# Kernel tuning notes

Hardware: AMD Instinct MI355X
Metric: run time of the kernel (lower is better)

The kernel has to match this reference:

```python
import jax, jax.numpy as jnp
import numpy as np

B, T, C = 2, 2048, 1024
N_HEAD = 16
HEAD_DIM = C // N_HEAD
ROPE_BASE = 10000.0


def setup_inputs() -> dict:
    key = jax.random.key(0)
    ks = jax.random.split(key, 5)
    s = 0.02
    return {
        "x": jax.random.normal(ks[0], (B, T, C), dtype=jnp.float32),
        "Wq": jax.random.normal(ks[1], (C, C), dtype=jnp.float32) * s,
        "Wk": jax.random.normal(ks[2], (C, C), dtype=jnp.float32) * s,
        "Wv": jax.random.normal(ks[3], (C, C), dtype=jnp.float32) * s,
        "Wo": jax.random.normal(ks[4], (C, C), dtype=jnp.float32) * s,
    }


def _rope_cos_sin(seq_len, head_dim, dtype):
    inv_freq = 1.0 / (ROPE_BASE ** (jnp.arange(0, head_dim, 2, dtype=jnp.float32) / head_dim))
    t = jnp.arange(seq_len, dtype=jnp.float32)
    freqs = jnp.einsum("i,j->ij", t, inv_freq)          # [T, head_dim/2]
    emb = jnp.concatenate([freqs, freqs], axis=-1)        # [T, head_dim]
    return jnp.cos(emb).astype(dtype), jnp.sin(emb).astype(dtype)


def _rotate_half(x):
    x1, x2 = jnp.split(x, 2, axis=-1)
    return jnp.concatenate([-x2, x1], axis=-1)


def _mha(x, Wq, Wk, Wv, Wo):
    b, t, c = x.shape
    # torch nn.Linear stores weight [out, in]: y = x @ W.T
    q = (x @ Wq.T).reshape(b, t, N_HEAD, HEAD_DIM).transpose(0, 2, 1, 3)  # [B,H,T,D]
    k = (x @ Wk.T).reshape(b, t, N_HEAD, HEAD_DIM).transpose(0, 2, 1, 3)
    v = (x @ Wv.T).reshape(b, t, N_HEAD, HEAD_DIM).transpose(0, 2, 1, 3)
    cos, sin = _rope_cos_sin(t, HEAD_DIM, x.dtype)        # [T,D] each, broadcast over B,H
    q = q * cos + _rotate_half(q) * sin
    k = k * cos + _rotate_half(k) * sin
    scale = 1.0 / np.sqrt(HEAD_DIM).astype(np.float32)
    att = jnp.einsum("bhqd,bhkd->bhqk", q, k) * scale     # [B,H,T,T]
    causal = jnp.tril(jnp.ones((t, t), dtype=bool))
    att = jnp.where(causal, att, jnp.finfo(att.dtype).min)
    att = jax.nn.softmax(att, axis=-1)
    y = jnp.einsum("bhqk,bhkd->bhqd", att, v)             # [B,H,T,D]
    y = y.transpose(0, 2, 1, 3).reshape(b, t, c)
    return y @ Wo.T


def reference(x, Wq, Wk, Wv, Wo):
    return _mha(x, Wq, Wk, Wv, Wo)
```

## Files before the change

kernel.cpp:

```cpp
#include <hip/hip_runtime.h>

#define BB 2
#define TT 2048
#define CC 1024
#define NH 16
#define HD 64

typedef __attribute__((ext_vector_type(8))) short bf16x8;
typedef __attribute__((ext_vector_type(4))) float floatx4;
typedef __attribute__((ext_vector_type(16))) float floatx16;

__device__ __forceinline__ unsigned short f2bf(float f) {
    union { float f; unsigned int u; } v; v.f = f;
    unsigned int u = v.u;
    u = (u + 0x7fffu + ((u >> 16) & 1u)) >> 16;
    return (unsigned short)u;
}
__device__ __forceinline__ float bf2f(unsigned short u) {
    return __uint_as_float((unsigned)u << 16);
}

typedef __attribute__((address_space(3))) unsigned char* lds_ptr_t;
typedef const __attribute__((address_space(1))) unsigned char* glob_ptr_t;
__device__ __forceinline__ void gll16(const void* g, void* l) {
    __builtin_amdgcn_global_load_lds((glob_ptr_t)g, (lds_ptr_t)l, 16, 0, 0);
}

__global__ __launch_bounds__(256) void cast_all_k(const float* __restrict__ x,
                                                  const float* __restrict__ wq,
                                                  const float* __restrict__ wk,
                                                  const float* __restrict__ wv,
                                                  const float* __restrict__ wo,
                                                  unsigned short* __restrict__ xb,
                                                  unsigned short* __restrict__ wqkvb,
                                                  unsigned short* __restrict__ wob,
                                                  float2* __restrict__ tabQ,
                                                  float2* __restrict__ tabK) {
    if (blockIdx.x >= 8192) {
        int idx = (blockIdx.x - 8192) * 256 + threadIdx.x;
        int t = idx >> 5, j = idx & 31;
        const float C1 = 0.41524101186092f;
        const float I2PI = 0.15915494309189535f;
        float rev = (float)t * (__builtin_amdgcn_exp2f(-(float)j * C1) * I2PI);
        rev -= floorf(rev);
        float ang = rev * 6.2831853071796f;
        float c = __cosf(ang), s = __sinf(ang);
        const float qs = 0.18033688011112f;
        tabK[idx] = make_float2(c, s);
        tabQ[idx] = make_float2(c * qs, s * qs);
        return;
    }
    int i = blockIdx.x * 256 + threadIdx.x;
    const float* src;
    unsigned short* dst;
    if (i < 1048576) {
        src = x + (size_t)i * 4;
        dst = xb + (size_t)i * 4;
    } else {
        int w   = (i - 1048576) >> 18;
        int off = (i - 1048576) & 262143;
        const float* s0 = (w == 0) ? wq : (w == 1) ? wk : (w == 2) ? wv : wo;
        unsigned short* d0 = (w == 3) ? wob : (wqkvb + (size_t)w * 1048576);
        src = s0 + (size_t)off * 4;
        dst = d0 + (size_t)off * 4;
    }
    float4 v = *(const float4*)src;
    ushort4 o;
    o.x = f2bf(v.x); o.y = f2bf(v.y); o.z = f2bf(v.z); o.w = f2bf(v.w);
    *(ushort4*)dst = o;
}

__global__ __launch_bounds__(256, 2) void gemm_o_k(const unsigned short* __restrict__ A,
                                                   const unsigned short* __restrict__ Bt,
                                                   float* __restrict__ C, int N, int K) {
    __shared__ __align__(16) unsigned short As[128][64];
    __shared__ __align__(16) unsigned short Bs[64][64];
    const int tid  = threadIdx.x;
    const int wave = tid >> 6;
    const int lane = tid & 63;
    const int quad = lane >> 4;
    const int l16  = lane & 15;
    const int sw   = l16 & 7;
    const int wr = (wave >> 1) * 64;
    const int wc = (wave & 1) * 32;
    const int bid = blockIdx.x;
    const int xcd = bid & 7, sl = bid >> 3;
    const int row0 = (xcd * 4 + (sl >> 4)) * 128;
    const int col0 = (sl & 15) * 64;
    const int w8r = wave * 8 + (lane >> 3);
    const int cg  = ((lane & 7) ^ (lane >> 3)) * 8;
    const int cl  = (lane & 7) * 8;

    const unsigned short* Ap = A  + (size_t)(row0 + w8r) * K + cg;
    const unsigned short* Bp = Bt + (size_t)(col0 + w8r) * K + cg;

    floatx4 acc[4][2];
    #pragma unroll
    for (int i = 0; i < 4; i++)
        #pragma unroll
        for (int j = 0; j < 2; j++) acc[i][j] = (floatx4){0.f, 0.f, 0.f, 0.f};

    for (int k0 = 0; k0 < K; k0 += 64) {
        __syncthreads();
        #pragma unroll
        for (int isu = 0; isu < 4; isu++)
            gll16(Ap + (size_t)(isu * 32) * K + k0, &As[isu * 32 + w8r][cl]);
        #pragma unroll
        for (int isu = 0; isu < 2; isu++)
            gll16(Bp + (size_t)(isu * 32) * K + k0, &Bs[isu * 32 + w8r][cl]);
        __syncthreads();
        #pragma unroll
        for (int kk = 0; kk < 2; kk++) {
            bf16x8 af[4], bfr[2];
            #pragma unroll
            for (int i = 0; i < 4; i++)
                af[i]  = *(const bf16x8*)&As[wr + 16 * i + l16][((kk * 4 + quad) ^ sw) * 8];
            #pragma unroll
            for (int j = 0; j < 2; j++)
                bfr[j] = *(const bf16x8*)&Bs[wc + 16 * j + l16][((kk * 4 + quad) ^ sw) * 8];
            #pragma unroll
            for (int i = 0; i < 4; i++)
                #pragma unroll
                for (int j = 0; j < 2; j++)
                    acc[i][j] = __builtin_amdgcn_mfma_f32_16x16x32_bf16(af[i], bfr[j], acc[i][j], 0, 0, 0);
        }
    }

    #pragma unroll
    for (int i = 0; i < 4; i++)
        #pragma unroll
        for (int j = 0; j < 2; j++)
            #pragma unroll
            for (int r = 0; r < 4; r++) {
                int row = row0 + wr + 16 * i + quad * 4 + r;
                int col = col0 + wc + 16 * j + l16;
                C[(size_t)row * N + col] = acc[i][j][r];
            }
}

__global__ __launch_bounds__(256) void gemm_qkv_k(const unsigned short* __restrict__ A,
                                                  const unsigned short* __restrict__ Bt,
                                                  const float2* __restrict__ tabQ,
                                                  const float2* __restrict__ tabK,
                                                  unsigned short* __restrict__ Qb,
                                                  unsigned short* __restrict__ Kb,
                                                  unsigned short* __restrict__ Vb) {
    __shared__ __align__(16) unsigned short SMEM[128 * 128];
    unsigned short (*As)[64] = (unsigned short(*)[64])SMEM;
    unsigned short (*Bs)[64] = (unsigned short(*)[64])(SMEM + 128 * 64);
    unsigned short (*Eb)[128] = (unsigned short(*)[128])SMEM;
    const int K = 1024;
    const int tid  = threadIdx.x;
    const int wave = tid >> 6;
    const int lane = tid & 63;
    const int quad = lane >> 4;
    const int l16  = lane & 15;
    const int sw   = l16 & 7;
    const int wr = (wave >> 1) * 64;
    const int wc = (wave & 1) * 64;
    const int bid = blockIdx.x;
    const int xcd = bid & 7, sl = bid >> 3;
    const int row0 = (xcd * 4 + sl / 24) * 128;
    const int col0 = (sl % 24) * 128;
    const int w8r = wave * 8 + (lane >> 3);
    const int cg  = ((lane & 7) ^ (lane >> 3)) * 8;
    const int cl  = (lane & 7) * 8;

    const unsigned short* Ap = A  + (size_t)(row0 + w8r) * K + cg;
    const unsigned short* Bp = Bt + (size_t)(col0 + w8r) * K + cg;

    floatx4 acc[4][4];
    #pragma unroll
    for (int i = 0; i < 4; i++)
        #pragma unroll
        for (int j = 0; j < 4; j++) acc[i][j] = (floatx4){0.f, 0.f, 0.f, 0.f};

    for (int k0 = 0; k0 < K; k0 += 64) {
        __syncthreads();
        #pragma unroll
        for (int isu = 0; isu < 4; isu++) {
            gll16(Ap + (size_t)(isu * 32) * K + k0, &As[isu * 32 + w8r][cl]);
            gll16(Bp + (size_t)(isu * 32) * K + k0, &Bs[isu * 32 + w8r][cl]);
        }
        __syncthreads();
        #pragma unroll
        for (int kk = 0; kk < 2; kk++) {
            bf16x8 af[4], bfr[4];
            #pragma unroll
            for (int i = 0; i < 4; i++)
                af[i]  = *(const bf16x8*)&As[wr + 16 * i + l16][((kk * 4 + quad) ^ sw) * 8];
            #pragma unroll
            for (int j = 0; j < 4; j++)
                bfr[j] = *(const bf16x8*)&Bs[wc + 16 * j + l16][((kk * 4 + quad) ^ sw) * 8];
            #pragma unroll
            for (int i = 0; i < 4; i++)
                #pragma unroll
                for (int j = 0; j < 4; j++)
                    acc[i][j] = __builtin_amdgcn_mfma_f32_16x16x32_bf16(af[i], bfr[j], acc[i][j], 0, 0, 0);
        }
    }

    __syncthreads();
    #pragma unroll
    for (int i = 0; i < 4; i++)
        #pragma unroll
        for (int j = 0; j < 4; j++)
            #pragma unroll
            for (int r = 0; r < 4; r++) {
                int erow = wr + 16 * i + quad * 4 + r;
                int col  = wc + 16 * j + l16;
                int pcol = (((col >> 3) ^ (erow & 15)) << 3) | (col & 7);
                Eb[erow][pcol] = f2bf(acc[i][j][r]);
            }
    __syncthreads();

    const int row  = tid >> 1;
    const int half = tid & 1;
    const int grow = row0 + row;
    const int t    = grow & (TT - 1);
    const int bb   = grow >> 11;
    const int sect = col0 >> 10;
    const int hh   = ((col0 & 1023) >> 6) + half;
    union { int4 q[8]; unsigned short u[64]; } raw;
    #pragma unroll
    for (int i = 0; i < 8; i++) {
        int pg = (half * 8 + i) ^ (row & 15);
        raw.q[i] = *(const int4*)&Eb[row][pg << 3];
    }
    size_t obase = ((size_t)(bb * NH + hh) * TT + t) * 64;
    if (sect == 2) {
        #pragma unroll
        for (int i = 0; i < 8; i++) *(int4*)(Vb + obase + 8 * i) = raw.q[i];
    } else {
        const float4* tab = (const float4*)((sect ? tabK : tabQ) + (size_t)t * 32);
        unsigned short* dst = sect ? Kb : Qb;
        union { int4 q[8]; unsigned short u[64]; } o;
        #pragma unroll
        for (int i = 0; i < 16; i++) {
            float4 cs = tab[i];
            int j0 = 2 * i, j1 = 2 * i + 1;
            float a0 = bf2f(raw.u[j0]), b0 = bf2f(raw.u[j0 + 32]);
            float a1 = bf2f(raw.u[j1]), b1 = bf2f(raw.u[j1 + 32]);
            o.u[j0]      = f2bf(a0 * cs.x - b0 * cs.y);
            o.u[j0 + 32] = f2bf(b0 * cs.x + a0 * cs.y);
            o.u[j1]      = f2bf(a1 * cs.z - b1 * cs.w);
            o.u[j1 + 32] = f2bf(b1 * cs.z + a1 * cs.w);
        }
        #pragma unroll
        for (int i = 0; i < 8; i++) *(int4*)(dst + obase + 8 * i) = o.q[i];
    }
}

__global__ __launch_bounds__(256) void vtr_k(const unsigned short* __restrict__ Vb,
                                             unsigned short* __restrict__ Vt) {
    __shared__ __align__(16) unsigned short Vsh[64][70];
    const int tid = threadIdx.x;
    const int tt = blockIdx.x;
    const int bh = blockIdx.y;
    const int sr = tid >> 2;
    const int sc = (tid & 3) * 16;
    const unsigned short* src = Vb + ((size_t)bh * TT + tt * 64 + sr) * 64 + sc;
    *(int4*)&Vsh[sr][sc]     = *(const int4*)src;
    *(int4*)&Vsh[sr][sc + 8] = *(const int4*)(src + 8);
    __syncthreads();
    const int dr = tid >> 2;
    const int tc = (tid & 3) * 16;
    unsigned short tv[16];
    #pragma unroll
    for (int i = 0; i < 16; i++) {
        int x = tc + i;
        int key = (x & ~15) + (x & 3) + ((x >> 2) & 1) * 8 + ((x >> 3) & 1) * 4;
        tv[i] = Vsh[key][dr];
    }
    size_t vo = ((size_t)bh * 64 + dr) * TT + tt * 64 + tc;
    *(int4*)(Vt + vo)     = *(int4*)&tv[0];
    *(int4*)(Vt + vo + 8) = *(int4*)&tv[8];
}

__global__ __launch_bounds__(256, 4) void flash_k(const unsigned short* __restrict__ Qb,
                                                  const unsigned short* __restrict__ Kb,
                                                  const unsigned short* __restrict__ Vt,
                                                  unsigned short* __restrict__ O0,
                                                  unsigned short* __restrict__ O1,
                                                  float* __restrict__ L0, float* __restrict__ L1) {
    __shared__ __align__(16) unsigned short Ks[64][72];
    __shared__ __align__(16) unsigned short Vs[64][72];
    const int tid  = threadIdx.x;
    const int wave = tid >> 6;
    const int lane = tid & 63;
    const int h    = lane >> 5;
    const int l32  = lane & 31;
    const int qt    = 15 - (blockIdx.x >> 6);
    const int inner = blockIdx.x & 63;
    const int bh    = inner >> 1;
    const int split = inner & 1;
    const int q0 = qt * 128;
    const int qw = q0 + wave * 32 + l32;
    const int sr = tid >> 2;
    const int sc = (tid & 3) * 16;

    bf16x8 qf[4];
    {
        const unsigned short* qp = Qb + ((size_t)bh * TT + qw) * 64 + h * 8;
        #pragma unroll
        for (int kk = 0; kk < 4; kk++) qf[kk] = *(const bf16x8*)(qp + kk * 16);
    }

    floatx16 accO[2];
    accO[0] = (floatx16)(0.f);
    accO[1] = (floatx16)(0.f);
    float lsum = 0.f;

    const int kt0 = split * (qt + 1);
    const int kt1 = kt0 + qt + 1;
    const unsigned short* kbase = Kb + (size_t)bh * TT * 64;
    const unsigned short* vbase = Vt + (size_t)bh * 64 * TT;

    const unsigned short* kp = kbase + ((size_t)(kt0 * 64) + sr) * 64 + sc;
    const unsigned short* vp = vbase + (size_t)sr * TT + kt0 * 64 + sc;
    int4 ka = *(const int4*)kp, kb2 = *(const int4*)(kp + 8);
    int4 va = *(const int4*)vp, vb2 = *(const int4*)(vp + 8);

    for (int kt = kt0; kt < kt1; kt++) {
        __syncthreads();
        *(int4*)&Ks[sr][sc]     = ka;
        *(int4*)&Ks[sr][sc + 8] = kb2;
        *(int4*)&Vs[sr][sc]     = va;
        *(int4*)&Vs[sr][sc + 8] = vb2;
        __syncthreads();
        if (kt + 1 < kt1) {
            const unsigned short* kp2 = kbase + ((size_t)((kt + 1) * 64) + sr) * 64 + sc;
            const unsigned short* vp2 = vbase + (size_t)sr * TT + (kt + 1) * 64 + sc;
            ka  = *(const int4*)kp2; kb2 = *(const int4*)(kp2 + 8);
            va  = *(const int4*)vp2; vb2 = *(const int4*)(vp2 + 8);
        }

        const bool diag = (kt >= 2 * qt);
        bf16x8 pfrag[4];

        #pragma unroll
        for (int mb = 0; mb < 2; mb++) {
            floatx16 sacc = (floatx16)(0.f);
            __builtin_amdgcn_s_setprio(1);
            #pragma unroll
            for (int kk = 0; kk < 4; kk++) {
                bf16x8 kf = *(const bf16x8*)&Ks[32 * mb + l32][kk * 16 + h * 8];
                sacc = __builtin_amdgcn_mfma_f32_32x32x16_bf16(kf, qf[kk], sacc, 0, 0, 0);
            }
            __builtin_amdgcn_s_setprio(0);
            float p[16];
            const int kmb = kt * 64 + 32 * mb + 4 * h;
            #pragma unroll
            for (int r = 0; r < 16; r++) {
                float pv = __builtin_amdgcn_exp2f(sacc[r]);
                if (diag) {
                    int ki = kmb + (r & 3) + 8 * (r >> 2);
                    if (ki > qw) pv = 0.f;
                }
                lsum += pv;
                p[r] = pv;
            }
            #pragma unroll
            for (int half = 0; half < 2; half++) {
                union { bf16x8 v; unsigned u[4]; } pk;
                #pragma unroll
                for (int i = 0; i < 4; i++) {
                    unsigned ulo = __float_as_uint(p[half * 8 + 2 * i]);
                    unsigned uhi = __float_as_uint(p[half * 8 + 2 * i + 1]);
                    pk.u[i] = (ulo >> 16) | (uhi & 0xffff0000u);
                }
                pfrag[2 * mb + half] = pk.v;
            }
        }

        __builtin_amdgcn_s_setprio(1);
        #pragma unroll
        for (int mbo = 0; mbo < 2; mbo++) {
            #pragma unroll
            for (int kk = 0; kk < 4; kk++) {
                bf16x8 vf = *(const bf16x8*)&Vs[32 * mbo + l32][kk * 16 + h * 8];
                accO[mbo] = __builtin_amdgcn_mfma_f32_32x32x16_bf16(vf, pfrag[kk], accO[mbo], 0, 0, 0);
            }
        }
        __builtin_amdgcn_s_setprio(0);
    }

    lsum += __shfl_xor(lsum, 32);
    unsigned short* Op = split ? O1 : O0;
    float* Lp = split ? L1 : L0;
    if (lane < 32) Lp[(size_t)bh * TT + qw] = lsum;
    unsigned short* orow = Op + ((size_t)bh * TT + qw) * 64;
    #pragma unroll
    for (int mbo = 0; mbo < 2; mbo++)
        #pragma unroll
        for (int a = 0; a < 4; a++) {
            ushort4 o4;
            o4.x = f2bf(accO[mbo][4 * a + 0]);
            o4.y = f2bf(accO[mbo][4 * a + 1]);
            o4.z = f2bf(accO[mbo][4 * a + 2]);
            o4.w = f2bf(accO[mbo][4 * a + 3]);
            *(ushort4*)(orow + 32 * mbo + 8 * a + 4 * h) = o4;
        }
}

__global__ __launch_bounds__(256) void combine_k(const unsigned short* __restrict__ O0,
                                                 const unsigned short* __restrict__ O1,
                                                 const float* __restrict__ L0,
                                                 const float* __restrict__ L1,
                                                 unsigned short* __restrict__ Yb) {
    int idx = blockIdx.x * 256 + threadIdx.x;
    int dg  = idx & 15;
    int row = idx >> 4;
    float inv = 1.0f / (L0[row] + L1[row]);
    uint2 a = ((const uint2*)O0)[idx];
    uint2 b = ((const uint2*)O1)[idx];
    float a0 = __uint_as_float(a.x << 16),      b0 = __uint_as_float(b.x << 16);
    float a1 = __uint_as_float(a.x & 0xffff0000u), b1 = __uint_as_float(b.x & 0xffff0000u);
    float a2 = __uint_as_float(a.y << 16),      b2 = __uint_as_float(b.y << 16);
    float a3 = __uint_as_float(a.y & 0xffff0000u), b3 = __uint_as_float(b.y & 0xffff0000u);
    ushort4 o;
    o.x = f2bf((a0 + b0) * inv);
    o.y = f2bf((a1 + b1) * inv);
    o.z = f2bf((a2 + b2) * inv);
    o.w = f2bf((a3 + b3) * inv);
    int bh = row >> 11, t = row & (TT - 1);
    int bb = bh >> 4, hh = bh & 15;
    *(ushort4*)(Yb + ((size_t)(bb * TT + t)) * CC + hh * 64 + dg * 4) = o;
}

extern "C" void kernel_launch(void* const* d_in, const int* in_sizes, int n_in,
                              void* d_out, int out_size, void* d_ws, size_t ws_size,
                              hipStream_t stream) {
    (void)in_sizes; (void)n_in; (void)out_size; (void)ws_size;
    const float* x  = (const float*)d_in[0];
    const float* Wq = (const float*)d_in[1];
    const float* Wk = (const float*)d_in[2];
    const float* Wv = (const float*)d_in[3];
    const float* Wo = (const float*)d_in[4];
    float* out = (float*)d_out;
    char* ws = (char*)d_ws;

    unsigned short* xb    = (unsigned short*)(ws + 0);
    unsigned short* wqkvb = (unsigned short*)(ws + (8ull  << 20));
    unsigned short* wob   = (unsigned short*)(ws + (14ull << 20));
    unsigned short* Qb    = (unsigned short*)(ws + (16ull << 20));
    unsigned short* Kb    = (unsigned short*)(ws + (24ull << 20));
    unsigned short* Vb    = (unsigned short*)(ws + (32ull << 20));
    unsigned short* Vt    = (unsigned short*)(ws + (40ull << 20));
    unsigned short* Yb    = (unsigned short*)(ws + (48ull << 20));
    unsigned short* O0    = (unsigned short*)(ws + (56ull << 20));
    unsigned short* O1    = (unsigned short*)(ws + (64ull << 20));
    float* L0 = (float*)(ws + (72ull << 20));
    float* L1 = (float*)(ws + (72ull << 20) + (256ull << 10));
    float2* tabQ = (float2*)(ws + (73ull << 20));
    float2* tabK = (float2*)(ws + (73ull << 20) + (512ull << 10));

    cast_all_k<<<8448, 256, 0, stream>>>(x, Wq, Wk, Wv, Wo, xb, wqkvb, wob, tabQ, tabK);
    gemm_qkv_k<<<768, 256, 0, stream>>>(xb, wqkvb, tabQ, tabK, Qb, Kb, Vb);
    vtr_k<<<dim3(32, 32), 256, 0, stream>>>(Vb, Vt);
    flash_k<<<1024, 256, 0, stream>>>(Qb, Kb, Vt, O0, O1, L0, L1);
    combine_k<<<4096, 256, 0, stream>>>(O0, O1, L0, L1, Yb);
    gemm_o_k<<<512, 256, 0, stream>>>(Yb, wob, out, 1024, 1024);
}
```

Measured before the change: 177.6 us.

## Double-buffer K/V tiles in flash kernel, use hardware bf16 pack, widen combine

The flash kernel now keeps two K/V shared-memory buffers. The next tile is written into the alternate buffer after the compute, so each iteration needs one barrier instead of two. P-fragment packing switches from truncation bit-masking to the v_cvt_pk_bf16_f32 instruction, which rounds instead of truncating. The combine kernel processes 8 bf16 elements per thread with 128-bit loads and stores, at half the grid size. Doubling LDS use (about 36KB per block) may reduce occupancy at launch bounds of 4 blocks.

```diff
diff --git a/kernel.cpp b/kernel.cpp
--- a/kernel.cpp
+++ b/kernel.cpp
@@ -283,8 +283,8 @@
                                                   unsigned short* __restrict__ O0,
                                                   unsigned short* __restrict__ O1,
                                                   float* __restrict__ L0, float* __restrict__ L1) {
-    __shared__ __align__(16) unsigned short Ks[64][72];
-    __shared__ __align__(16) unsigned short Vs[64][72];
+    __shared__ __align__(16) unsigned short Ks[2][64][72];
+    __shared__ __align__(16) unsigned short Vs[2][64][72];
     const int tid  = threadIdx.x;
     const int wave = tid >> 6;
     const int lane = tid & 63;
@@ -316,19 +316,23 @@
     const unsigned short* kbase = Kb + (size_t)bh * TT * 64;
     const unsigned short* vbase = Vt + (size_t)bh * 64 * TT;
 
-    const unsigned short* kp = kbase + ((size_t)(kt0 * 64) + sr) * 64 + sc;
-    const unsigned short* vp = vbase + (size_t)sr * TT + kt0 * 64 + sc;
-    int4 ka = *(const int4*)kp, kb2 = *(const int4*)(kp + 8);
-    int4 va = *(const int4*)vp, vb2 = *(const int4*)(vp + 8);
-
+    {
+        const unsigned short* kp = kbase + ((size_t)(kt0 * 64) + sr) * 64 + sc;
+        const unsigned short* vp = vbase + (size_t)sr * TT + kt0 * 64 + sc;
+        int4 ka = *(const int4*)kp, kb2 = *(const int4*)(kp + 8);
+        int4 va = *(const int4*)vp, vb2 = *(const int4*)(vp + 8);
+        *(int4*)&Ks[0][sr][sc]     = ka;
+        *(int4*)&Ks[0][sr][sc + 8] = kb2;
+        *(int4*)&Vs[0][sr][sc]     = va;
+        *(int4*)&Vs[0][sr][sc + 8] = vb2;
+    }
+    __syncthreads();
+
+    int cur = 0;
     for (int kt = kt0; kt < kt1; kt++) {
-        __syncthreads();
-        *(int4*)&Ks[sr][sc]     = ka;
-        *(int4*)&Ks[sr][sc + 8] = kb2;
-        *(int4*)&Vs[sr][sc]     = va;
-        *(int4*)&Vs[sr][sc + 8] = vb2;
-        __syncthreads();
-        if (kt + 1 < kt1) {
+        int4 ka, kb2, va, vb2;
+        const bool more = (kt + 1 < kt1);
+        if (more) {
             const unsigned short* kp2 = kbase + ((size_t)((kt + 1) * 64) + sr) * 64 + sc;
             const unsigned short* vp2 = vbase + (size_t)sr * TT + (kt + 1) * 64 + sc;
             ka  = *(const int4*)kp2; kb2 = *(const int4*)(kp2 + 8);
@@ -344,30 +348,31 @@
             __builtin_amdgcn_s_setprio(1);
             #pragma unroll
             for (int kk = 0; kk < 4; kk++) {
-                bf16x8 kf = *(const bf16x8*)&Ks[32 * mb + l32][kk * 16 + h * 8];
+                bf16x8 kf = *(const bf16x8*)&Ks[cur][32 * mb + l32][kk * 16 + h * 8];
                 sacc = __builtin_amdgcn_mfma_f32_32x32x16_bf16(kf, qf[kk], sacc, 0, 0, 0);
             }
             __builtin_amdgcn_s_setprio(0);
-            float p[16];
             const int kmb = kt * 64 + 32 * mb + 4 * h;
             #pragma unroll
-            for (int r = 0; r < 16; r++) {
-                float pv = __builtin_amdgcn_exp2f(sacc[r]);
-                if (diag) {
-                    int ki = kmb + (r & 3) + 8 * (r >> 2);
-                    if (ki > qw) pv = 0.f;
+            for (int half = 0; half < 2; half++) {
+                float p[8];
+                #pragma unroll
+                for (int rr = 0; rr < 8; rr++) {
+                    int r = half * 8 + rr;
+                    float pv = __builtin_amdgcn_exp2f(sacc[r]);
+                    if (diag) {
+                        int ki = kmb + (r & 3) + 8 * (r >> 2);
+                        if (ki > qw) pv = 0.f;
+                    }
+                    lsum += pv;
+                    p[rr] = pv;
                 }
-                lsum += pv;
-                p[r] = pv;
-            }
-            #pragma unroll
-            for (int half = 0; half < 2; half++) {
                 union { bf16x8 v; unsigned u[4]; } pk;
                 #pragma unroll
                 for (int i = 0; i < 4; i++) {
-                    unsigned ulo = __float_as_uint(p[half * 8 + 2 * i]);
-                    unsigned uhi = __float_as_uint(p[half * 8 + 2 * i + 1]);
-                    pk.u[i] = (ulo >> 16) | (uhi & 0xffff0000u);
+                    unsigned r;
+                    asm("v_cvt_pk_bf16_f32 %0, %1, %2" : "=v"(r) : "v"(p[2 * i]), "v"(p[2 * i + 1]));
+                    pk.u[i] = r;
                 }
                 pfrag[2 * mb + half] = pk.v;
             }
@@ -378,11 +383,20 @@
         for (int mbo = 0; mbo < 2; mbo++) {
             #pragma unroll
             for (int kk = 0; kk < 4; kk++) {
-                bf16x8 vf = *(const bf16x8*)&Vs[32 * mbo + l32][kk * 16 + h * 8];
+                bf16x8 vf = *(const bf16x8*)&Vs[cur][32 * mbo + l32][kk * 16 + h * 8];
                 accO[mbo] = __builtin_amdgcn_mfma_f32_32x32x16_bf16(vf, pfrag[kk], accO[mbo], 0, 0, 0);
             }
         }
         __builtin_amdgcn_s_setprio(0);
+
+        if (more) {
+            *(int4*)&Ks[cur ^ 1][sr][sc]     = ka;
+            *(int4*)&Ks[cur ^ 1][sr][sc + 8] = kb2;
+            *(int4*)&Vs[cur ^ 1][sr][sc]     = va;
+            *(int4*)&Vs[cur ^ 1][sr][sc + 8] = vb2;
+        }
+        __syncthreads();
+        cur ^= 1;
     }
 
     lsum += __shfl_xor(lsum, 32);
@@ -409,23 +423,28 @@
                                                  const float* __restrict__ L1,
                                                  unsigned short* __restrict__ Yb) {
     int idx = blockIdx.x * 256 + threadIdx.x;
-    int dg  = idx & 15;
-    int row = idx >> 4;
+    int dg  = idx & 7;
+    int row = idx >> 3;
     float inv = 1.0f / (L0[row] + L1[row]);
-    uint2 a = ((const uint2*)O0)[idx];
-    uint2 b = ((const uint2*)O1)[idx];
-    float a0 = __uint_as_float(a.x << 16),      b0 = __uint_as_float(b.x << 16);
-    float a1 = __uint_as_float(a.x & 0xffff0000u), b1 = __uint_as_float(b.x & 0xffff0000u);
-    float a2 = __uint_as_float(a.y << 16),      b2 = __uint_as_float(b.y << 16);
-    float a3 = __uint_as_float(a.y & 0xffff0000u), b3 = __uint_as_float(b.y & 0xffff0000u);
-    ushort4 o;
-    o.x = f2bf((a0 + b0) * inv);
-    o.y = f2bf((a1 + b1) * inv);
-    o.z = f2bf((a2 + b2) * inv);
-    o.w = f2bf((a3 + b3) * inv);
+    uint4 a = ((const uint4*)O0)[idx];
+    uint4 b = ((const uint4*)O1)[idx];
+    unsigned au[4] = {a.x, a.y, a.z, a.w};
+    unsigned bu[4] = {b.x, b.y, b.z, b.w};
+    unsigned ou[4];
+    #pragma unroll
+    for (int i = 0; i < 4; i++) {
+        float alo = __uint_as_float(au[i] << 16), blo = __uint_as_float(bu[i] << 16);
+        float ahi = __uint_as_float(au[i] & 0xffff0000u), bhi = __uint_as_float(bu[i] & 0xffff0000u);
+        float rlo = (alo + blo) * inv;
+        float rhi = (ahi + bhi) * inv;
+        unsigned r;
+        asm("v_cvt_pk_bf16_f32 %0, %1, %2" : "=v"(r) : "v"(rlo), "v"(rhi));
+        ou[i] = r;
+    }
     int bh = row >> 11, t = row & (TT - 1);
     int bb = bh >> 4, hh = bh & 15;
-    *(ushort4*)(Yb + ((size_t)(bb * TT + t)) * CC + hh * 64 + dg * 4) = o;
+    uint4 o = make_uint4(ou[0], ou[1], ou[2], ou[3]);
+    *(uint4*)(Yb + ((size_t)(bb * TT + t)) * CC + hh * 64 + dg * 8) = o;
 }
 
 extern "C" void kernel_launch(void* const* d_in, const int* in_sizes, int n_in,
@@ -459,6 +478,6 @@
     gemm_qkv_k<<<768, 256, 0, stream>>>(xb, wqkvb, tabQ, tabK, Qb, Kb, Vb);
     vtr_k<<<dim3(32, 32), 256, 0, stream>>>(Vb, Vt);
     flash_k<<<1024, 256, 0, stream>>>(Qb, Kb, Vt, O0, O1, L0, L1);
-    combine_k<<<4096, 256, 0, stream>>>(O0, O1, L0, L1, Yb);
+    combine_k<<<2048, 256, 0, stream>>>(O0, O1, L0, L1, Yb);
     gemm_o_k<<<512, 256, 0, stream>>>(Yb, wob, out, 1024, 1024);
 }
```

Measured after the change: 181.5 us. 1.02x slower.

## Drop split-KV flash attention and fuse normalization into flash epilogue

Applied to the files above, without the earlier changes.

Removes the two-way key split of the flash kernel, so each block walks the full causal key range for its query tile and writes normalized bf16 output straight into Yb. This eliminates the combine kernel and the partial O/L round trip through memory. The cost is half as many blocks (512), with longer and less even per-block work, which may leave CUs underused for the short diagonal tiles.

```diff
diff --git a/kernel.cpp b/kernel.cpp
--- a/kernel.cpp
+++ b/kernel.cpp
@@ -280,9 +280,7 @@
 __global__ __launch_bounds__(256, 4) void flash_k(const unsigned short* __restrict__ Qb,
                                                   const unsigned short* __restrict__ Kb,
                                                   const unsigned short* __restrict__ Vt,
-                                                  unsigned short* __restrict__ O0,
-                                                  unsigned short* __restrict__ O1,
-                                                  float* __restrict__ L0, float* __restrict__ L1) {
+                                                  unsigned short* __restrict__ Yb) {
     __shared__ __align__(16) unsigned short Ks[64][72];
     __shared__ __align__(16) unsigned short Vs[64][72];
     const int tid  = threadIdx.x;
@@ -290,10 +288,8 @@
     const int lane = tid & 63;
     const int h    = lane >> 5;
     const int l32  = lane & 31;
-    const int qt    = 15 - (blockIdx.x >> 6);
-    const int inner = blockIdx.x & 63;
-    const int bh    = inner >> 1;
-    const int split = inner & 1;
+    const int qt   = 15 - (blockIdx.x >> 5);
+    const int bh   = blockIdx.x & 31;
     const int q0 = qt * 128;
     const int qw = q0 + wave * 32 + l32;
     const int sr = tid >> 2;
@@ -311,17 +307,16 @@
     accO[1] = (floatx16)(0.f);
     float lsum = 0.f;
 
-    const int kt0 = split * (qt + 1);
-    const int kt1 = kt0 + qt + 1;
+    const int kt1 = 2 * qt + 2;
     const unsigned short* kbase = Kb + (size_t)bh * TT * 64;
     const unsigned short* vbase = Vt + (size_t)bh * 64 * TT;
 
-    const unsigned short* kp = kbase + ((size_t)(kt0 * 64) + sr) * 64 + sc;
-    const unsigned short* vp = vbase + (size_t)sr * TT + kt0 * 64 + sc;
+    const unsigned short* kp = kbase + (size_t)sr * 64 + sc;
+    const unsigned short* vp = vbase + (size_t)sr * TT + sc;
     int4 ka = *(const int4*)kp, kb2 = *(const int4*)(kp + 8);
     int4 va = *(const int4*)vp, vb2 = *(const int4*)(vp + 8);
 
-    for (int kt = kt0; kt < kt1; kt++) {
+    for (int kt = 0; kt < kt1; kt++) {
         __syncthreads();
         *(int4*)&Ks[sr][sc]     = ka;
         *(int4*)&Ks[sr][sc + 8] = kb2;
@@ -386,46 +381,20 @@
     }
 
     lsum += __shfl_xor(lsum, 32);
-    unsigned short* Op = split ? O1 : O0;
-    float* Lp = split ? L1 : L0;
-    if (lane < 32) Lp[(size_t)bh * TT + qw] = lsum;
-    unsigned short* orow = Op + ((size_t)bh * TT + qw) * 64;
+    const float inv = 1.0f / lsum;
+    const int bb = bh >> 4, hh = bh & 15;
+    unsigned short* orow = Yb + ((size_t)(bb * TT + qw)) * CC + hh * 64;
     #pragma unroll
     for (int mbo = 0; mbo < 2; mbo++)
         #pragma unroll
         for (int a = 0; a < 4; a++) {
             ushort4 o4;
-            o4.x = f2bf(accO[mbo][4 * a + 0]);
-            o4.y = f2bf(accO[mbo][4 * a + 1]);
-            o4.z = f2bf(accO[mbo][4 * a + 2]);
-            o4.w = f2bf(accO[mbo][4 * a + 3]);
+            o4.x = f2bf(accO[mbo][4 * a + 0] * inv);
+            o4.y = f2bf(accO[mbo][4 * a + 1] * inv);
+            o4.z = f2bf(accO[mbo][4 * a + 2] * inv);
+            o4.w = f2bf(accO[mbo][4 * a + 3] * inv);
             *(ushort4*)(orow + 32 * mbo + 8 * a + 4 * h) = o4;
         }
-}
-
-__global__ __launch_bounds__(256) void combine_k(const unsigned short* __restrict__ O0,
-                                                 const unsigned short* __restrict__ O1,
-                                                 const float* __restrict__ L0,
-                                                 const float* __restrict__ L1,
-                                                 unsigned short* __restrict__ Yb) {
-    int idx = blockIdx.x * 256 + threadIdx.x;
-    int dg  = idx & 15;
-    int row = idx >> 4;
-    float inv = 1.0f / (L0[row] + L1[row]);
-    uint2 a = ((const uint2*)O0)[idx];
-    uint2 b = ((const uint2*)O1)[idx];
-    float a0 = __uint_as_float(a.x << 16),      b0 = __uint_as_float(b.x << 16);
-    float a1 = __uint_as_float(a.x & 0xffff0000u), b1 = __uint_as_float(b.x & 0xffff0000u);
-    float a2 = __uint_as_float(a.y << 16),      b2 = __uint_as_float(b.y << 16);
-    float a3 = __uint_as_float(a.y & 0xffff0000u), b3 = __uint_as_float(b.y & 0xffff0000u);
-    ushort4 o;
-    o.x = f2bf((a0 + b0) * inv);
-    o.y = f2bf((a1 + b1) * inv);
-    o.z = f2bf((a2 + b2) * inv);
-    o.w = f2bf((a3 + b3) * inv);
-    int bh = row >> 11, t = row & (TT - 1);
-    int bb = bh >> 4, hh = bh & 15;
-    *(ushort4*)(Yb + ((size_t)(bb * TT + t)) * CC + hh * 64 + dg * 4) = o;
 }
 
 extern "C" void kernel_launch(void* const* d_in, const int* in_sizes, int n_in,
@@ -448,17 +417,12 @@
     unsigned short* Vb    = (unsigned short*)(ws + (32ull << 20));
     unsigned short* Vt    = (unsigned short*)(ws + (40ull << 20));
     unsigned short* Yb    = (unsigned short*)(ws + (48ull << 20));
-    unsigned short* O0    = (unsigned short*)(ws + (56ull << 20));
-    unsigned short* O1    = (unsigned short*)(ws + (64ull << 20));
-    float* L0 = (float*)(ws + (72ull << 20));
-    float* L1 = (float*)(ws + (72ull << 20) + (256ull << 10));
     float2* tabQ = (float2*)(ws + (73ull << 20));
     float2* tabK = (float2*)(ws + (73ull << 20) + (512ull << 10));
 
     cast_all_k<<<8448, 256, 0, stream>>>(x, Wq, Wk, Wv, Wo, xb, wqkvb, wob, tabQ, tabK);
     gemm_qkv_k<<<768, 256, 0, stream>>>(xb, wqkvb, tabQ, tabK, Qb, Kb, Vb);
     vtr_k<<<dim3(32, 32), 256, 0, stream>>>(Vb, Vt);
-    flash_k<<<1024, 256, 0, stream>>>(Qb, Kb, Vt, O0, O1, L0, L1);
-    combine_k<<<4096, 256, 0, stream>>>(O0, O1, L0, L1, Yb);
+    flash_k<<<512, 256, 0, stream>>>(Qb, Kb, Vt, Yb);
     gemm_o_k<<<512, 256, 0, stream>>>(Yb, wob, out, 1024, 1024);
 }
```

After: 186.8 us. 1.05x slower.
